# Optimization experiments

Measured on AMD Instinct MI355X. Metric: run time of the kernel, lower is better.

The kernel has to match this reference:

```python
import jax, jax.numpy as jnp
import numpy as np

N_NODES = 50000
N_EDGES = 600000
IN_DIM = 128
OUT_DIM = 128
N_REL = 32
N_BASES = 4
BN_EPS = 1e-5


def setup_inputs() -> dict:
    key = jax.random.key(0)
    ks = jax.random.split(key, 8)
    entity_emb = jax.random.normal(ks[0], (N_NODES, IN_DIM), dtype=jnp.float32)
    bases = jax.random.normal(ks[1], (N_BASES, IN_DIM, OUT_DIM), dtype=jnp.float32) * 0.05
    coefficients = jax.random.normal(ks[2], (N_REL, N_BASES), dtype=jnp.float32) * 0.5
    W_loop = jax.random.normal(ks[3], (IN_DIM, OUT_DIM), dtype=jnp.float32) * 0.05
    b_loop = jnp.zeros((OUT_DIM,), dtype=jnp.float32)
    gamma = jnp.ones((OUT_DIM,), dtype=jnp.float32)
    beta = jnp.zeros((OUT_DIM,), dtype=jnp.float32)
    edge_index = jax.random.randint(ks[4], (2, N_EDGES), 0, N_NODES, dtype=jnp.int32)
    edge_type = jax.random.randint(ks[5], (N_EDGES,), 0, N_REL, dtype=jnp.int32)
    return {"entity_emb": entity_emb, "bases": bases, "coefficients": coefficients,
            "W_loop": W_loop, "b_loop": b_loop, "gamma": gamma, "beta": beta,
            "edge_index": edge_index, "edge_type": edge_type}


def reference(entity_emb, bases, coefficients, W_loop, b_loop, gamma, beta, edge_index, edge_type):
    N = entity_emb.shape[0]
    # self-loop linear
    out = entity_emb @ W_loop + b_loop  # [N, out_dim]
    # basis decomposition: per-relation weight W[r] = sum_b coeff[r,b] * bases[b]
    W = jnp.einsum('rb,bio->rio', coefficients, bases)  # [R, in, out]
    src, dst = edge_index[0], edge_index[1]
    # per-edge message: entity_emb[src_e] @ W[edge_type_e]  (vectorizes the per-relation loop)
    msg = jnp.einsum('ei,eio->eo', entity_emb[src], W[edge_type])  # [E, out]
    out = out + jax.ops.segment_sum(msg, dst, num_segments=N)
    # degree normalization (in-degree over all edges, clamped at 1)
    deg = jax.ops.segment_sum(jnp.ones_like(dst, dtype=out.dtype), dst, num_segments=N)
    out = out / jnp.maximum(deg, 1.0)[:, None]
    # BatchNorm1d (training mode: biased batch stats over node dim)
    mean = jnp.mean(out, axis=0)
    var = jnp.mean((out - mean) ** 2, axis=0)
    out = (out - mean) / jnp.sqrt(var + BN_EPS) * gamma + beta
    return jax.nn.relu(out)
```

## Files before the change

### kernel.cpp

```cpp
#include <hip/hip_runtime.h>
#include <cstdint>

#define NN 50000
#define NE 600000
#define NPAIRS 1563
#define GSTRIDE 512

typedef unsigned short ushort_t;
typedef __bf16 bf16_t;
typedef __attribute__((ext_vector_type(8))) bf16_t bf16x8;
typedef __attribute__((ext_vector_type(8))) ushort_t ushort8;
typedef __attribute__((ext_vector_type(4))) float f32x4;

#define WT_OFF   0ul
#define XG_OFF   40960ul
#define XBF_OFF  16040960ul
#define CNT_OFF  19240960ul
#define CUR_OFF  19290960ul
#define BSUM_OFF 19340960ul
#define BSCN_OFF 19341088ul
#define CS_OFF   19341216ul
#define CSQ_OFF  19341344ul

__device__ __forceinline__ float2 bf2_to_f2(uint32_t u) {
    float2 r;
    r.x = __uint_as_float(u << 16);
    r.y = __uint_as_float(u & 0xffff0000u);
    return r;
}

__device__ __forceinline__ ushort_t f2bf(float f) {
    uint32_t u = __float_as_uint(f);
    u = (u + 0x7fffu + ((u >> 16) & 1u)) >> 16;
    return (ushort_t)u;
}

__device__ __forceinline__ uint32_t f2bf2(float x, float y) {
    return (uint32_t)f2bf(x) | ((uint32_t)f2bf(y) << 16);
}

__device__ __forceinline__ void async_copy16(const void* g, void* l) {
    __builtin_amdgcn_global_load_lds(
        (const __attribute__((address_space(1))) void*)g,
        (__attribute__((address_space(3))) void*)l, 16, 0, 0);
}

__global__ __launch_bounds__(256) void k_prep(
    const float* __restrict__ Wl, const float* __restrict__ bases,
    ushort_t* __restrict__ WT)
{
    const int i = blockIdx.x * 256 + threadIdx.x;
    if (i >= 128 * 640) return;
    const int n = i / 640;
    const int kk = i - n * 640;
    float v;
    if (kk < 128) v = Wl[kk * 128 + n];
    else {
        const int j = kk - 128;
        v = bases[(size_t)(j >> 7) * 16384 + (j & 127) * 128 + n];
    }
    WT[i] = f2bf(v);
}

__global__ __launch_bounds__(256) void k_cast(
    const float* __restrict__ X, ushort_t* __restrict__ Xbf,
    ushort_t* __restrict__ XG)
{
    __shared__ ushort_t L[16][136];
    const int tid = threadIdx.x;
    const int tile = blockIdx.x;
    {
        const int row = tid >> 4, gc = tid & 15;
        const int node = tile * 16 + row;
        const float4* p = (const float4*)(X + (size_t)node * 128 + gc * 8);
        const float4 a = p[0], b = p[1];
        ushort_t t8[8] = { f2bf(a.x), f2bf(a.y), f2bf(a.z), f2bf(a.w),
                           f2bf(b.x), f2bf(b.y), f2bf(b.z), f2bf(b.w) };
        const uint4 v = *(const uint4*)t8;
        *(uint4*)&L[row][gc * 8] = v;
        *(uint4*)(Xbf + (size_t)node * 128 + gc * 8) = v;
    }
    __syncthreads();
    {
        const int g = tid >> 4, r2 = tid & 15;
        const uint4 u = *(const uint4*)&L[r2][g * 8];
        *(uint4*)(XG + (size_t)tile * 10240 + g * 128 + r2 * 8) = u;
    }
}

__global__ __launch_bounds__(256) void k_hist(
    const int* __restrict__ eidx, int* __restrict__ cnt)
{
    const int* __restrict__ dst = eidx + NE;
    for (int e = blockIdx.x * 256 + threadIdx.x; e < NE; e += gridDim.x * 256)
        atomicAdd(cnt + dst[e], 1);
}

__global__ __launch_bounds__(256) void k_scan1(
    const int* __restrict__ cnt, int* __restrict__ curs, int* __restrict__ bsum)
{
    __shared__ int sh[256];
    const int tid = threadIdx.x;
    const int i0 = blockIdx.x * 512 + tid * 2;
    const int v0 = (i0 < NN) ? cnt[i0] : 0;
    const int v1 = (i0 + 1 < NN) ? cnt[i0 + 1] : 0;
    int s = v0 + v1;
    sh[tid] = s;
    __syncthreads();
#pragma unroll
    for (int off = 1; off < 256; off <<= 1) {
        int t = (tid >= off) ? sh[tid - off] : 0;
        __syncthreads();
        sh[tid] += t;
        __syncthreads();
    }
    const int excl = sh[tid] - s;
    if (i0 < NN) curs[i0] = excl;
    if (i0 + 1 < NN) curs[i0 + 1] = excl + v0;
    if (tid == 255) bsum[blockIdx.x] = sh[255];
}

__global__ __launch_bounds__(128) void k_scan2(
    const int* __restrict__ bsum, int* __restrict__ bscan, int nblk)
{
    __shared__ int sh[128];
    const int tid = threadIdx.x;
    int v = (tid < nblk) ? bsum[tid] : 0;
    sh[tid] = v;
    __syncthreads();
#pragma unroll
    for (int off = 1; off < 128; off <<= 1) {
        int t = (tid >= off) ? sh[tid - off] : 0;
        __syncthreads();
        sh[tid] += t;
        __syncthreads();
    }
    if (tid < nblk) bscan[tid] = sh[tid] - v;
}

__global__ __launch_bounds__(256) void k_scan3(
    int* __restrict__ curs, const int* __restrict__ bscan)
{
    const int add = bscan[blockIdx.x];
    const int i0 = blockIdx.x * 512 + threadIdx.x * 2;
    if (i0 < NN) curs[i0] += add;
    if (i0 + 1 < NN) curs[i0 + 1] += add;
}

__global__ __launch_bounds__(256) void k_scatter(
    const int* __restrict__ eidx, const int* __restrict__ etype,
    int* __restrict__ curs, uint32_t* __restrict__ epack)
{
    const int* __restrict__ src = eidx;
    const int* __restrict__ dst = eidx + NE;
    for (int e = blockIdx.x * 256 + threadIdx.x; e < NE; e += gridDim.x * 256) {
        const int d = dst[e];
        const int pos = atomicAdd(curs + d, 1);
        epack[pos] = (uint32_t)src[e] | ((uint32_t)etype[e] << 16);
    }
}

__device__ __forceinline__ void edge_accum8(
    uint32_t ep, const ushort_t* __restrict__ Xbf,
    const float* __restrict__ coeff, int k, float* m)
{
    const int s = ep & 0xffff;
    const int t = ep >> 16;
    const float4 cw = *(const float4*)(coeff + t * 4);
    const uint4 xv = *(const uint4*)(Xbf + (size_t)s * 128 + k * 8);
    float x[8];
    float2 p;
    p = bf2_to_f2(xv.x); x[0] = p.x; x[1] = p.y;
    p = bf2_to_f2(xv.y); x[2] = p.x; x[3] = p.y;
    p = bf2_to_f2(xv.z); x[4] = p.x; x[5] = p.y;
    p = bf2_to_f2(xv.w); x[6] = p.x; x[7] = p.y;
#pragma unroll
    for (int c = 0; c < 8; ++c) {
        m[0 * 8 + c] += cw.x * x[c];
        m[1 * 8 + c] += cw.y * x[c];
        m[2 * 8 + c] += cw.z * x[c];
        m[3 * 8 + c] += cw.w * x[c];
    }
}

__global__ __launch_bounds__(256) void k_gather(
    const ushort_t* __restrict__ Xbf, const uint32_t* __restrict__ epack,
    const int* __restrict__ cnt, const int* __restrict__ curs,
    const float* __restrict__ coeff, ushort_t* __restrict__ XG)
{
    const int lane = threadIdx.x & 63;
    const int w = threadIdx.x >> 6;
    const int sub = lane >> 4;
    const int k = lane & 15;
    const int tile = blockIdx.x;
    const int d = tile * 16 + w * 4 + sub;

    const int n = cnt[d];
    const int end = curs[d];
    int j = end - n;

    float m[32];
#pragma unroll
    for (int i = 0; i < 32; ++i) m[i] = 0.f;

    for (; j + 3 < end; j += 4) {
        const uint32_t e0 = epack[j];
        const uint32_t e1 = epack[j + 1];
        const uint32_t e2 = epack[j + 2];
        const uint32_t e3 = epack[j + 3];
        edge_accum8(e0, Xbf, coeff, k, m);
        edge_accum8(e1, Xbf, coeff, k, m);
        edge_accum8(e2, Xbf, coeff, k, m);
        edge_accum8(e3, Xbf, coeff, k, m);
    }
    for (; j < end; ++j) edge_accum8(epack[j], Xbf, coeff, k, m);

    uint32_t* gb = (uint32_t*)(XG + (size_t)tile * 10240);
#pragma unroll
    for (int b = 0; b < 4; ++b) {
        uint4 v;
        v.x = f2bf2(m[b * 8 + 0], m[b * 8 + 1]);
        v.y = f2bf2(m[b * 8 + 2], m[b * 8 + 3]);
        v.z = f2bf2(m[b * 8 + 4], m[b * 8 + 5]);
        v.w = f2bf2(m[b * 8 + 6], m[b * 8 + 7]);
        *(uint4*)(gb + (16 + b * 16 + k) * 64 + (w * 4 + sub) * 4) = v;
    }
}

__global__ __launch_bounds__(256, 2) void k_gemm_f(
    const ushort_t* __restrict__ XG, const ushort_t* __restrict__ WT,
    const float* __restrict__ bl, const int* __restrict__ cnt,
    float* __restrict__ out, float* __restrict__ colsum,
    float* __restrict__ colsq)
{
    __shared__ ushort_t As[2][2][10240];
    const int tid = threadIdx.x;
    const int lane = tid & 63;
    const int w = tid >> 6;
    const int m = lane & 15;
    const int quad = lane >> 4;

    auto stage = [&](int buf, int pr) {
        const ushort_t* base = XG + (size_t)pr * 20480;
#pragma unroll
        for (int j = 0; j < 10; ++j) {
            const int idx = w * 10 + j;
            const int tl = idx / 20;
            const int off = idx - tl * 20;
            async_copy16(base + (size_t)tl * 10240 + off * 512 + lane * 8,
                         &As[buf][tl][off * 512]);
        }
    };

    int p = blockIdx.x;
    stage(0, p);

    const ushort_t* bp0 = WT + (size_t)(w * 32 + m) * 640 + quad * 8;
    const ushort_t* bp1 = bp0 + 16 * 640;
    ushort8 B0[20], B1[20];
#pragma unroll
    for (int c = 0; c < 20; ++c) {
        B0[c] = *(const ushort8*)(bp0 + c * 32);
        B1[c] = *(const ushort8*)(bp1 + c * 32);
    }
    const float blv0 = bl[w * 32 + m];
    const float blv1 = bl[w * 32 + 16 + m];
    float s0 = 0.f, q0 = 0.f, s1 = 0.f, q1 = 0.f;

    __syncthreads();

    int buf = 0;
    while (p < NPAIRS) {
        const int pn = p + GSTRIDE;
        if (pn < NPAIRS) stage(buf ^ 1, pn);

        f32x4 cc[2][2];
#pragma unroll
        for (int rt = 0; rt < 2; ++rt)
#pragma unroll
            for (int ct = 0; ct < 2; ++ct)
#pragma unroll
                for (int i = 0; i < 4; ++i) cc[rt][ct][i] = 0.f;

#pragma unroll
        for (int c = 0; c < 20; ++c) {
            const int aoff = (c * 4 + quad) * 128 + m * 8;
            const bf16x8 a0 = __builtin_bit_cast(bf16x8, *(const ushort8*)&As[buf][0][aoff]);
            const bf16x8 a1 = __builtin_bit_cast(bf16x8, *(const ushort8*)&As[buf][1][aoff]);
            const bf16x8 b0 = __builtin_bit_cast(bf16x8, B0[c]);
            const bf16x8 b1 = __builtin_bit_cast(bf16x8, B1[c]);
            cc[0][0] = __builtin_amdgcn_mfma_f32_16x16x32_bf16(a0, b0, cc[0][0], 0, 0, 0);
            cc[0][1] = __builtin_amdgcn_mfma_f32_16x16x32_bf16(a0, b1, cc[0][1], 0, 0, 0);
            cc[1][0] = __builtin_amdgcn_mfma_f32_16x16x32_bf16(a1, b0, cc[1][0], 0, 0, 0);
            cc[1][1] = __builtin_amdgcn_mfma_f32_16x16x32_bf16(a1, b1, cc[1][1], 0, 0, 0);
        }

        const int row0 = p * 32;
#pragma unroll
        for (int rt = 0; rt < 2; ++rt) {
            const int rowb = row0 + rt * 16 + quad * 4;
#pragma unroll
            for (int r = 0; r < 4; ++r) {
                const int row = rowb + r;
                if (row < NN) {
                    const int dg = cnt[row];
                    const float inv = 1.0f / (float)((dg > 0) ? dg : 1);
                    float* po = out + (size_t)row * 128 + w * 32 + m;
                    const float v0 = (cc[rt][0][r] + blv0) * inv;
                    const float v1 = (cc[rt][1][r] + blv1) * inv;
                    po[0]  = v0;
                    po[16] = v1;
                    s0 += v0; q0 += v0 * v0;
                    s1 += v1; q1 += v1 * v1;
                }
            }
        }

        if (pn < NPAIRS) __syncthreads();
        buf ^= 1;
        p = pn;
    }

    s0 += __shfl_down(s0, 32); q0 += __shfl_down(q0, 32);
    s0 += __shfl_down(s0, 16); q0 += __shfl_down(q0, 16);
    s1 += __shfl_down(s1, 32); q1 += __shfl_down(q1, 32);
    s1 += __shfl_down(s1, 16); q1 += __shfl_down(q1, 16);
    if (lane < 16) {
        atomicAdd(colsum + w * 32 + lane, s0);
        atomicAdd(colsq  + w * 32 + lane, q0);
        atomicAdd(colsum + w * 32 + 16 + lane, s1);
        atomicAdd(colsq  + w * 32 + 16 + lane, q1);
    }
}

__global__ __launch_bounds__(256) void k_bn_relu(
    float* __restrict__ out, const float* __restrict__ colsum,
    const float* __restrict__ colsq, const float* __restrict__ gamma,
    const float* __restrict__ beta)
{
    __shared__ float sc[128], sh[128];
    const int tid = threadIdx.x;
    if (tid < 128) {
        const float mean = colsum[tid] * (1.0f / NN);
        const float var = colsq[tid] * (1.0f / NN) - mean * mean;
        const float g = gamma[tid] * rsqrtf(var + 1e-5f);
        sc[tid] = g;
        sh[tid] = beta[tid] - mean * g;
    }
    __syncthreads();
    const int total = NN * 32;
    for (int i = blockIdx.x * 256 + tid; i < total; i += gridDim.x * 256) {
        const int c = (i & 31) << 2;
        float4 v = *(float4*)(out + (size_t)i * 4);
        v.x = fmaxf(fmaf(v.x, sc[c + 0], sh[c + 0]), 0.f);
        v.y = fmaxf(fmaf(v.y, sc[c + 1], sh[c + 1]), 0.f);
        v.z = fmaxf(fmaf(v.z, sc[c + 2], sh[c + 2]), 0.f);
        v.w = fmaxf(fmaf(v.w, sc[c + 3], sh[c + 3]), 0.f);
        *(float4*)(out + (size_t)i * 4) = v;
    }
}

extern "C" void kernel_launch(void* const* d_in, const int* in_sizes, int n_in,
                              void* d_out, int out_size, void* d_ws, size_t ws_size,
                              hipStream_t stream)
{
    const float* X      = (const float*)d_in[0];
    const float* bases  = (const float*)d_in[1];
    const float* coeff  = (const float*)d_in[2];
    const float* Wl     = (const float*)d_in[3];
    const float* bl     = (const float*)d_in[4];
    const float* gamma  = (const float*)d_in[5];
    const float* beta   = (const float*)d_in[6];
    const int*   eidx   = (const int*)d_in[7];
    const int*   etype  = (const int*)d_in[8];
    float* out = (float*)d_out;

    float* ws = (float*)d_ws;
    ushort_t* WT     = (ushort_t*)(ws + WT_OFF);
    ushort_t* XG     = (ushort_t*)(ws + XG_OFF);
    ushort_t* Xbf    = (ushort_t*)(ws + XBF_OFF);
    int*      cnt    = (int*)(ws + CNT_OFF);
    int*      curs   = (int*)(ws + CUR_OFF);
    int*      bsum   = (int*)(ws + BSUM_OFF);
    int*      bscan  = (int*)(ws + BSCN_OFF);
    float*    colsum = ws + CS_OFF;
    float*    colsq  = ws + CSQ_OFF;
    uint32_t* epack  = (uint32_t*)d_out;

    hipMemsetAsync(cnt, 0, (CSQ_OFF + 128 - CNT_OFF) * sizeof(float), stream);

    const int nblk_scan = (NN + 511) / 512;

    k_prep<<<(128 * 640 + 255) / 256, 256, 0, stream>>>(Wl, bases, WT);
    k_cast<<<3125, 256, 0, stream>>>(X, Xbf, XG);
    k_hist<<<2048, 256, 0, stream>>>(eidx, cnt);
    k_scan1<<<nblk_scan, 256, 0, stream>>>(cnt, curs, bsum);
    k_scan2<<<1, 128, 0, stream>>>(bsum, bscan, nblk_scan);
    k_scan3<<<nblk_scan, 256, 0, stream>>>(curs, bscan);
    k_scatter<<<2048, 256, 0, stream>>>(eidx, etype, curs, epack);
    k_gather<<<3125, 256, 0, stream>>>(Xbf, epack, cnt, curs, coeff, XG);
    k_gemm_f<<<GSTRIDE, 256, 0, stream>>>(XG, WT, bl, cnt, out, colsum, colsq);
    k_bn_relu<<<1024, 256, 0, stream>>>(out, colsum, colsq, gamma, beta);
}
```

Measured before the change: 256.9 us.

## Fuse edge gather into GEMM kernel, writing aggregated features directly to LDS

The per-destination basis-coefficient gather moves inside the GEMM kernel. Each block now accumulates edge messages for its 32 nodes and writes them as bf16 straight into shared memory with an XOR swizzle, so the 16 MB XG intermediate is no longer written to and re-read from global memory. Only the self-loop features are staged asynchronously, and the LDS buffer is halved by dropping double buffering. The cost is that the irregular gather now sits on the GEMM's critical path with no overlap against the next tile's staging. The gather also runs at only 2 blocks per CU with a heavy register footprint, which may cut its latency hiding.

```diff
diff --git a/kernel.cpp b/kernel.cpp
--- a/kernel.cpp
+++ b/kernel.cpp
@@ -13,14 +13,15 @@
 typedef __attribute__((ext_vector_type(4))) float f32x4;
 
 #define WT_OFF   0ul
-#define XG_OFF   40960ul
-#define XBF_OFF  16040960ul
-#define CNT_OFF  19240960ul
-#define CUR_OFF  19290960ul
-#define BSUM_OFF 19340960ul
-#define BSCN_OFF 19341088ul
-#define CS_OFF   19341216ul
-#define CSQ_OFF  19341344ul
+#define XGX_OFF  40960ul
+#define XBF_OFF  3240960ul
+#define EPK_OFF  6440960ul
+#define CNT_OFF  7040960ul
+#define CUR_OFF  7090960ul
+#define BSUM_OFF 7140960ul
+#define BSCN_OFF 7141088ul
+#define CS_OFF   7141216ul
+#define CSQ_OFF  7141344ul
 
 __device__ __forceinline__ float2 bf2_to_f2(uint32_t u) {
     float2 r;
@@ -64,7 +65,7 @@
 
 __global__ __launch_bounds__(256) void k_cast(
     const float* __restrict__ X, ushort_t* __restrict__ Xbf,
-    ushort_t* __restrict__ XG)
+    ushort_t* __restrict__ XGX)
 {
     __shared__ ushort_t L[16][136];
     const int tid = threadIdx.x;
@@ -84,7 +85,7 @@
     {
         const int g = tid >> 4, r2 = tid & 15;
         const uint4 u = *(const uint4*)&L[r2][g * 8];
-        *(uint4*)(XG + (size_t)tile * 10240 + g * 128 + r2 * 8) = u;
+        *(uint4*)(XGX + (size_t)tile * 2048 + g * 128 + r2 * 8) = u;
     }
 }
 
@@ -183,77 +184,21 @@
     }
 }
 
-__global__ __launch_bounds__(256) void k_gather(
+__global__ __launch_bounds__(256, 2) void k_gemm_f(
+    const ushort_t* __restrict__ XGX, const ushort_t* __restrict__ WT,
     const ushort_t* __restrict__ Xbf, const uint32_t* __restrict__ epack,
+    const float* __restrict__ coeff, const float* __restrict__ bl,
     const int* __restrict__ cnt, const int* __restrict__ curs,
-    const float* __restrict__ coeff, ushort_t* __restrict__ XG)
-{
-    const int lane = threadIdx.x & 63;
-    const int w = threadIdx.x >> 6;
-    const int sub = lane >> 4;
-    const int k = lane & 15;
-    const int tile = blockIdx.x;
-    const int d = tile * 16 + w * 4 + sub;
-
-    const int n = cnt[d];
-    const int end = curs[d];
-    int j = end - n;
-
-    float m[32];
-#pragma unroll
-    for (int i = 0; i < 32; ++i) m[i] = 0.f;
-
-    for (; j + 3 < end; j += 4) {
-        const uint32_t e0 = epack[j];
-        const uint32_t e1 = epack[j + 1];
-        const uint32_t e2 = epack[j + 2];
-        const uint32_t e3 = epack[j + 3];
-        edge_accum8(e0, Xbf, coeff, k, m);
-        edge_accum8(e1, Xbf, coeff, k, m);
-        edge_accum8(e2, Xbf, coeff, k, m);
-        edge_accum8(e3, Xbf, coeff, k, m);
-    }
-    for (; j < end; ++j) edge_accum8(epack[j], Xbf, coeff, k, m);
-
-    uint32_t* gb = (uint32_t*)(XG + (size_t)tile * 10240);
-#pragma unroll
-    for (int b = 0; b < 4; ++b) {
-        uint4 v;
-        v.x = f2bf2(m[b * 8 + 0], m[b * 8 + 1]);
-        v.y = f2bf2(m[b * 8 + 2], m[b * 8 + 3]);
-        v.z = f2bf2(m[b * 8 + 4], m[b * 8 + 5]);
-        v.w = f2bf2(m[b * 8 + 6], m[b * 8 + 7]);
-        *(uint4*)(gb + (16 + b * 16 + k) * 64 + (w * 4 + sub) * 4) = v;
-    }
-}
-
-__global__ __launch_bounds__(256, 2) void k_gemm_f(
-    const ushort_t* __restrict__ XG, const ushort_t* __restrict__ WT,
-    const float* __restrict__ bl, const int* __restrict__ cnt,
     float* __restrict__ out, float* __restrict__ colsum,
     float* __restrict__ colsq)
 {
-    __shared__ ushort_t As[2][2][10240];
+    __shared__ ushort_t As[2][10240];
     const int tid = threadIdx.x;
     const int lane = tid & 63;
     const int w = tid >> 6;
     const int m = lane & 15;
     const int quad = lane >> 4;
-
-    auto stage = [&](int buf, int pr) {
-        const ushort_t* base = XG + (size_t)pr * 20480;
-#pragma unroll
-        for (int j = 0; j < 10; ++j) {
-            const int idx = w * 10 + j;
-            const int tl = idx / 20;
-            const int off = idx - tl * 20;
-            async_copy16(base + (size_t)tl * 10240 + off * 512 + lane * 8,
-                         &As[buf][tl][off * 512]);
-        }
-    };
-
-    int p = blockIdx.x;
-    stage(0, p);
+    const int w4s = w * 4 + quad;
 
     const ushort_t* bp0 = WT + (size_t)(w * 32 + m) * 640 + quad * 8;
     const ushort_t* bp1 = bp0 + 16 * 640;
@@ -267,12 +212,55 @@
     const float blv1 = bl[w * 32 + 16 + m];
     float s0 = 0.f, q0 = 0.f, s1 = 0.f, q1 = 0.f;
 
-    __syncthreads();
-
-    int buf = 0;
+    int p = blockIdx.x;
     while (p < NPAIRS) {
-        const int pn = p + GSTRIDE;
-        if (pn < NPAIRS) stage(buf ^ 1, pn);
+        {
+            const size_t tb = (size_t)p * 4096;
+#pragma unroll
+            for (int j = 0; j < 2; ++j) {
+                const int idx = w * 2 + j;
+                const int tl = idx >> 2;
+                const int off = idx & 3;
+                const int G = off * 4 + quad;
+                const int r = m ^ G;
+                async_copy16(XGX + tb + (size_t)tl * 2048 + G * 128 + r * 8,
+                             &As[tl][off * 512 + lane * 8]);
+            }
+        }
+
+        for (int tl = 0; tl < 2; ++tl) {
+            const int d = p * 32 + tl * 16 + w4s;
+            int n = 0, end = 0;
+            if (d < NN) { n = cnt[d]; end = curs[d]; }
+            int j = end - n;
+            float mm[32];
+#pragma unroll
+            for (int i = 0; i < 32; ++i) mm[i] = 0.f;
+            for (; j + 3 < end; j += 4) {
+                const uint32_t e0 = epack[j];
+                const uint32_t e1 = epack[j + 1];
+                const uint32_t e2 = epack[j + 2];
+                const uint32_t e3 = epack[j + 3];
+                edge_accum8(e0, Xbf, coeff, m, mm);
+                edge_accum8(e1, Xbf, coeff, m, mm);
+                edge_accum8(e2, Xbf, coeff, m, mm);
+                edge_accum8(e3, Xbf, coeff, m, mm);
+            }
+            for (; j < end; ++j) edge_accum8(epack[j], Xbf, coeff, m, mm);
+
+#pragma unroll
+            for (int b = 0; b < 4; ++b) {
+                uint4 v;
+                v.x = f2bf2(mm[b * 8 + 0], mm[b * 8 + 1]);
+                v.y = f2bf2(mm[b * 8 + 2], mm[b * 8 + 3]);
+                v.z = f2bf2(mm[b * 8 + 4], mm[b * 8 + 5]);
+                v.w = f2bf2(mm[b * 8 + 6], mm[b * 8 + 7]);
+                *(uint4*)&As[tl][(size_t)(16 + b * 16 + m) * 128 +
+                                 (size_t)(w4s ^ m) * 8] = v;
+            }
+        }
+
+        __syncthreads();
 
         f32x4 cc[2][2];
 #pragma unroll
@@ -284,9 +272,10 @@
 
 #pragma unroll
         for (int c = 0; c < 20; ++c) {
-            const int aoff = (c * 4 + quad) * 128 + m * 8;
-            const bf16x8 a0 = __builtin_bit_cast(bf16x8, *(const ushort8*)&As[buf][0][aoff]);
-            const bf16x8 a1 = __builtin_bit_cast(bf16x8, *(const ushort8*)&As[buf][1][aoff]);
+            const int g = c * 4 + quad;
+            const int aoff = g * 128 + ((m ^ (g & 15)) * 8);
+            const bf16x8 a0 = __builtin_bit_cast(bf16x8, *(const ushort8*)&As[0][aoff]);
+            const bf16x8 a1 = __builtin_bit_cast(bf16x8, *(const ushort8*)&As[1][aoff]);
             const bf16x8 b0 = __builtin_bit_cast(bf16x8, B0[c]);
             const bf16x8 b1 = __builtin_bit_cast(bf16x8, B1[c]);
             cc[0][0] = __builtin_amdgcn_mfma_f32_16x16x32_bf16(a0, b0, cc[0][0], 0, 0, 0);
@@ -316,9 +305,8 @@
             }
         }
 
-        if (pn < NPAIRS) __syncthreads();
-        buf ^= 1;
-        p = pn;
+        p += GSTRIDE;
+        if (p < NPAIRS) __syncthreads();
     }
 
     s0 += __shfl_down(s0, 32); q0 += __shfl_down(q0, 32);
@@ -377,28 +365,28 @@
 
     float* ws = (float*)d_ws;
     ushort_t* WT     = (ushort_t*)(ws + WT_OFF);
-    ushort_t* XG     = (ushort_t*)(ws + XG_OFF);
+    ushort_t* XGX    = (ushort_t*)(ws + XGX_OFF);
     ushort_t* Xbf    = (ushort_t*)(ws + XBF_OFF);
+    uint32_t* epack  = (uint32_t*)(ws + EPK_OFF);
     int*      cnt    = (int*)(ws + CNT_OFF);
     int*      curs   = (int*)(ws + CUR_OFF);
     int*      bsum   = (int*)(ws + BSUM_OFF);
     int*      bscan  = (int*)(ws + BSCN_OFF);
     float*    colsum = ws + CS_OFF;
     float*    colsq  = ws + CSQ_OFF;
-    uint32_t* epack  = (uint32_t*)d_out;
 
     hipMemsetAsync(cnt, 0, (CSQ_OFF + 128 - CNT_OFF) * sizeof(float), stream);
 
     const int nblk_scan = (NN + 511) / 512;
 
     k_prep<<<(128 * 640 + 255) / 256, 256, 0, stream>>>(Wl, bases, WT);
-    k_cast<<<3125, 256, 0, stream>>>(X, Xbf, XG);
+    k_cast<<<3125, 256, 0, stream>>>(X, Xbf, XGX);
     k_hist<<<2048, 256, 0, stream>>>(eidx, cnt);
     k_scan1<<<nblk_scan, 256, 0, stream>>>(cnt, curs, bsum);
     k_scan2<<<1, 128, 0, stream>>>(bsum, bscan, nblk_scan);
     k_scan3<<<nblk_scan, 256, 0, stream>>>(curs, bscan);
     k_scatter<<<2048, 256, 0, stream>>>(eidx, etype, curs, epack);
-    k_gather<<<3125, 256, 0, stream>>>(Xbf, epack, cnt, curs, coeff, XG);
-    k_gemm_f<<<GSTRIDE, 256, 0, stream>>>(XG, WT, bl, cnt, out, colsum, colsq);
+    k_gemm_f<<<GSTRIDE, 256, 0, stream>>>(XGX, WT, Xbf, epack, coeff, bl,
+                                          cnt, curs, out, colsum, colsq);
     k_bn_relu<<<1024, 256, 0, stream>>>(out, colsum, colsq, gamma, beta);
 }
```

After: 275.7 us. 1.07x slower.
